# Kernel tuning notes

Hardware: AMD Instinct MI355X
Metric: run time of the kernel (lower is better)

Reference implementation:

```python
import jax, jax.numpy as jnp
import numpy as np

BETA = 0.25
N_E = 1024
E_DIM = 64
B, L = 32, 2048


def setup_inputs() -> dict:
    key = jax.random.key(0)
    k1, k2 = jax.random.split(key)
    z = jax.random.normal(k1, (B, L, E_DIM), dtype=jnp.float32)
    # torch init: uniform_(-1/n_e, 1/n_e)
    codebook = jax.random.uniform(k2, (N_E, E_DIM), dtype=jnp.float32,
                                  minval=-1.0 / N_E, maxval=1.0 / N_E)
    return {"z": z, "codebook": codebook}


def reference(z, codebook):
    sg = jax.lax.stop_gradient
    n_e = codebook.shape[0]
    zf = z.reshape(-1, codebook.shape[1])  # (N, e_dim)
    # squared-distance matrix: ||z||^2 + ||e||^2 - 2 z.e  -> (N, n_e)
    d = (jnp.sum(zf * zf, axis=1, keepdims=True)
         + jnp.sum(codebook * codebook, axis=1)
         - 2.0 * zf @ codebook.T)
    idx = jnp.argmin(d, axis=1)  # (N,)
    # one-hot @ codebook is just a gather
    z_q = codebook[idx].reshape(z.shape)
    loss = (jnp.mean((sg(z_q) - z) ** 2)
            + BETA * jnp.mean((z_q - sg(z)) ** 2))
    # straight-through estimator
    z_q_st = z + sg(z_q - z)
    # codebook usage stats (mean of one-hot rows == normalized histogram)
    counts = jnp.zeros((n_e,), dtype=z.dtype).at[idx].add(1.0)
    e_mean = counts / idx.shape[0]
    perplexity = jnp.exp(-jnp.sum(e_mean * jnp.log(e_mean + 1e-10)))
    return loss, z_q_st, perplexity, idx
```

## Files before the change

kernel.cpp:

```cpp
#include <hip/hip_runtime.h>
#include <math.h>

#define E_DIM 64
#define N_E   1024
#define BETA  0.25
#define NROWS 65536

using bf16x8 = __attribute__((ext_vector_type(8))) short;
using f32x4  = __attribute__((ext_vector_type(4))) float;
#define MFMA(a, b, c) __builtin_amdgcn_mfma_f32_16x16x32_bf16((a), (b), (c), 0, 0, 0)


__device__ __forceinline__ unsigned short f2bf_rn(float f) {
    unsigned u = __builtin_bit_cast(unsigned, f);
    unsigned r = u + 0x7fffu + ((u >> 16) & 1u);
    return (unsigned short)(r >> 16);
}
__device__ __forceinline__ float bf2f(unsigned short b) {
    unsigned u = ((unsigned)b) << 16;
    return __builtin_bit_cast(float, u);
}

__device__ __forceinline__ float pw64_sq(const float* v) {
    float r[8];
#pragma unroll
    for (int l = 0; l < 8; ++l) r[l] = v[l] * v[l];
#pragma unroll
    for (int t = 1; t < 8; ++t)
#pragma unroll
        for (int l = 0; l < 8; ++l) r[l] += v[8 * t + l] * v[8 * t + l];
    return ((r[0] + r[1]) + (r[2] + r[3])) + ((r[4] + r[5]) + (r[6] + r[7]));
}

__global__ __launch_bounds__(256) void k_prep(const float* __restrict__ cb,
                                              unsigned short* __restrict__ ebh,
                                              unsigned short* __restrict__ ebl,
                                              float* __restrict__ h,
                                              unsigned* __restrict__ hist,
                                              double* __restrict__ sse,
                                              unsigned* __restrict__ flagN) {
    int t = blockIdx.x * 256 + threadIdx.x;
    {
        int e = t & 7, lane = (t >> 3) & 63, ks = (t >> 9) & 1, ct = t >> 10;
        int j = ct * 16 + (lane & 15);
        int k = ks * 32 + ((lane >> 4) << 3) + e;
        float v = cb[j * 64 + k];
        unsigned short hi = f2bf_rn(v);
        ebh[t] = hi;
        ebl[t] = f2bf_rn(v - bf2f(hi));
    }
    if (blockIdx.x < 4) {
        int j = t;
        float e[E_DIM];
        const float4* ep = reinterpret_cast<const float4*>(cb + (size_t)j * E_DIM);
#pragma unroll
        for (int k4 = 0; k4 < E_DIM / 4; ++k4) {
            float4 v = ep[k4];
            e[4 * k4 + 0] = v.x; e[4 * k4 + 1] = v.y;
            e[4 * k4 + 2] = v.z; e[4 * k4 + 3] = v.w;
        }
        h[j] = pw64_sq(e);
    } else if (blockIdx.x == 4) {
#pragma unroll
        for (int u = 0; u < 4; ++u) hist[threadIdx.x * 4 + u] = 0u;
    } else if (blockIdx.x == 5 && threadIdx.x == 0) {
        *sse = 0.0;
        *flagN = 0u;
    }
}

__global__ __launch_bounds__(512, 4) void k_mfma(
    const float* __restrict__ z, const float* __restrict__ cb,
    const float* __restrict__ h,
    const unsigned short* __restrict__ ebh, const unsigned short* __restrict__ ebl,
    float* __restrict__ out_zq, float* __restrict__ out_idx,
    unsigned* __restrict__ hist, double* __restrict__ sse,
    unsigned* __restrict__ flagN, unsigned* __restrict__ flagL) {
    const int lane = threadIdx.x & 63;
    const int w = __builtin_amdgcn_readfirstlane(threadIdx.x >> 6);
    const int m = lane & 15, g = lane >> 4;
    const int half = w >> 2;
    const int rw   = w & 3;

    __shared__ int bok;
    __shared__ float rsv[128];
    __shared__ float sb0[2][128], sb1[2][128];
    __shared__ int   sbi[2][128];
    __shared__ float wp[8];
    if (threadIdx.x == 0) bok = 1;
    __syncthreads();

    {
        bf16x8 a, b;
#pragma unroll
        for (int e = 0; e < 8; ++e) {
            int k = g * 8 + e;
            a[e] = (short)f2bf_rn((float)(((m * 3 + k * 7) & 15) - 7));
            b[e] = (short)f2bf_rn((float)(((k * 5 + m * 3) & 15) - 8));
        }
        f32x4 acc = {0.f, 0.f, 0.f, 0.f};
        acc = MFMA(a, b, acc);
        bool ok = true;
#pragma unroll
        for (int r = 0; r < 4; ++r) {
            int rr = g * 4 + r;
            float E = 0.f;
            for (int k = 0; k < 32; ++k)
                E += (float)((((rr * 3 + k * 7) & 15) - 7) * (((k * 5 + m * 3) & 15) - 8));
            ok = ok && (acc[r] == E);
        }
        if (!ok) atomicAnd(&bok, 0);
    }
    __syncthreads();
    if (!bok) {
        if (threadIdx.x < 128) {
            unsigned p = atomicAdd(flagN, 1u);
            flagL[p] = (unsigned)(blockIdx.x * 128 + threadIdx.x);
        }
        return;
    }

    const int rowb32 = blockIdx.x * 128 + rw * 32;
    bf16x8 a0h0, a0l0, a0h1, a0l1, a1h0, a1l0, a1h1, a1l1;
#define ALOAD(P, AH0, AL0, AH1, AL1) {                                         \
        const int rowA = rowb32 + (P) * 16 + m;                                \
        const float4* zr = reinterpret_cast<const float4*>(z + (size_t)rowA * 64); \
        float4 p0 = zr[g * 2], p1 = zr[g * 2 + 1];                             \
        float4 p2 = zr[8 + g * 2], p3 = zr[9 + g * 2];                         \
        float t0[8] = {p0.x, p0.y, p0.z, p0.w, p1.x, p1.y, p1.z, p1.w};        \
        float t1[8] = {p2.x, p2.y, p2.z, p2.w, p3.x, p3.y, p3.z, p3.w};        \
        float s = 0.f;                                                         \
        _Pragma("unroll")                                                      \
        for (int e = 0; e < 8; ++e) {                                          \
            s += fabsf(t0[e]) + fabsf(t1[e]);                                  \
            float x0 = 2.0f * t0[e]; unsigned short h0 = f2bf_rn(x0);          \
            AH0[e] = (short)h0; AL0[e] = (short)f2bf_rn(x0 - bf2f(h0));        \
            float x1 = 2.0f * t1[e]; unsigned short h1 = f2bf_rn(x1);          \
            AH1[e] = (short)h1; AL1[e] = (short)f2bf_rn(x1 - bf2f(h1));        \
        }                                                                      \
        s += __shfl_xor(s, 16);                                                \
        s += __shfl_xor(s, 32);                                                \
        if (g == 0 && half == 0) rsv[rw * 32 + (P) * 16 + m] = s;              \
    }
    ALOAD(0, a0h0, a0l0, a0h1, a0l1)
    ALOAD(1, a1h0, a1l0, a1h1, a1l1)
#undef ALOAD

    float bb00 = INFINITY, bb01 = INFINITY, bb02 = INFINITY, bb03 = INFINITY;
    float bb10 = INFINITY, bb11 = INFINITY, bb12 = INFINITY, bb13 = INFINITY;
    float ss00 = INFINITY, ss01 = INFINITY, ss02 = INFINITY, ss03 = INFINITY;
    float ss10 = INFINITY, ss11 = INFINITY, ss12 = INFINITY, ss13 = INFINITY;
    int   ii00 = 0, ii01 = 0, ii02 = 0, ii03 = 0;
    int   ii10 = 0, ii11 = 0, ii12 = 0, ii13 = 0;
#define UPD(S, B0, B1, I0) { float _s = (S);                                   \
        if (_s < B0) { B1 = B0; B0 = _s; I0 = j; } else B1 = fminf(B1, _s); }

    const bf16x8* pBh = reinterpret_cast<const bf16x8*>(ebh);
    const bf16x8* pBl = reinterpret_cast<const bf16x8*>(ebl);
    const int ct0 = half * 32;

    bf16x8 Ah0 = pBh[ct0 * 128 + lane],        Ah1 = pBh[ct0 * 128 + lane + 64];
    bf16x8 Al0 = pBl[ct0 * 128 + lane],        Al1 = pBl[ct0 * 128 + lane + 64];
    bf16x8 Bh0 = pBh[(ct0 + 1) * 128 + lane],  Bh1 = pBh[(ct0 + 1) * 128 + lane + 64];
    bf16x8 Bl0 = pBl[(ct0 + 1) * 128 + lane],  Bl1 = pBl[(ct0 + 1) * 128 + lane + 64];

#define COLTILE(CT, VH0, VH1, VL0, VL1) {                                      \
        const int j = (CT) * 16 + m;                                           \
        const float hj = h[j];                                                 \
        const f32x4 z4 = {0.f, 0.f, 0.f, 0.f};                                 \
        f32x4 s0 = MFMA(a0h0, VH0, z4);                                        \
        f32x4 s1 = MFMA(a1h0, VH0, z4);                                        \
        s0 = MFMA(a0h1, VH1, s0);                                              \
        s1 = MFMA(a1h1, VH1, s1);                                              \
        s0 = MFMA(a0h0, VL0, s0);                                              \
        s1 = MFMA(a1h0, VL0, s1);                                              \
        s0 = MFMA(a0h1, VL1, s0);                                              \
        s1 = MFMA(a1h1, VL1, s1);                                              \
        s0 = MFMA(a0l0, VH0, s0);                                              \
        s1 = MFMA(a1l0, VH0, s1);                                              \
        s0 = MFMA(a0l1, VH1, s0);                                              \
        s1 = MFMA(a1l1, VH1, s1);                                              \
        UPD(hj - s0[0], bb00, ss00, ii00)                                      \
        UPD(hj - s0[1], bb01, ss01, ii01)                                      \
        UPD(hj - s0[2], bb02, ss02, ii02)                                      \
        UPD(hj - s0[3], bb03, ss03, ii03)                                      \
        UPD(hj - s1[0], bb10, ss10, ii10)                                      \
        UPD(hj - s1[1], bb11, ss11, ii11)                                      \
        UPD(hj - s1[2], bb12, ss12, ii12)                                      \
        UPD(hj - s1[3], bb13, ss13, ii13)                                      \
    }

#pragma unroll 1
    for (int ct = ct0; ct < ct0 + 32; ct += 2) {
        COLTILE(ct, Ah0, Ah1, Al0, Al1);
        if (ct + 2 < ct0 + 32) {
            const int fb = (ct + 2) * 128 + lane;
            Ah0 = pBh[fb]; Ah1 = pBh[fb + 64];
            Al0 = pBl[fb]; Al1 = pBl[fb + 64];
        }
        COLTILE(ct + 1, Bh0, Bh1, Bl0, Bl1);
        if (ct + 3 < ct0 + 32) {
            const int fb = (ct + 3) * 128 + lane;
            Bh0 = pBh[fb]; Bh1 = pBh[fb + 64];
            Bl0 = pBl[fb]; Bl1 = pBl[fb + 64];
        }
    }
#undef COLTILE
#undef UPD

#pragma unroll
    for (int mask = 1; mask < 16; mask <<= 1) {
#define MRG(B0, I0, B1) { float ob0 = __shfl_xor(B0, mask); int oi = __shfl_xor(I0, mask); \
        float ob1 = __shfl_xor(B1, mask); \
        if (ob0 < B0) { B1 = fminf(fminf(B0, B1), ob1); B0 = ob0; I0 = oi; } \
        else { B1 = fminf(B1, fminf(ob0, ob1)); } }
        MRG(bb00, ii00, ss00) MRG(bb01, ii01, ss01)
        MRG(bb02, ii02, ss02) MRG(bb03, ii03, ss03)
        MRG(bb10, ii10, ss10) MRG(bb11, ii11, ss11)
        MRG(bb12, ii12, ss12) MRG(bb13, ii13, ss13)
#undef MRG
    }

    if (m == 0) {
        const int r0 = rw * 32 + g * 4;
        sb0[half][r0 + 0] = bb00; sb1[half][r0 + 0] = ss00; sbi[half][r0 + 0] = ii00;
        sb0[half][r0 + 1] = bb01; sb1[half][r0 + 1] = ss01; sbi[half][r0 + 1] = ii01;
        sb0[half][r0 + 2] = bb02; sb1[half][r0 + 2] = ss02; sbi[half][r0 + 2] = ii02;
        sb0[half][r0 + 3] = bb03; sb1[half][r0 + 3] = ss03; sbi[half][r0 + 3] = ii03;
        const int r1 = r0 + 16;
        sb0[half][r1 + 0] = bb10; sb1[half][r1 + 0] = ss10; sbi[half][r1 + 0] = ii10;
        sb0[half][r1 + 1] = bb11; sb1[half][r1 + 1] = ss11; sbi[half][r1 + 1] = ii11;
        sb0[half][r1 + 2] = bb12; sb1[half][r1 + 2] = ss12; sbi[half][r1 + 2] = ii12;
        sb0[half][r1 + 3] = bb13; sb1[half][r1 + 3] = ss13; sbi[half][r1 + 3] = ii13;
    }
    __syncthreads();

    {
        const int rloc = threadIdx.x >> 2, q = threadIdx.x & 3;
        const int rowO = blockIdx.x * 128 + rloc;
        float b0 = sb0[0][rloc], b1 = sb1[0][rloc];
        int   vi = sbi[0][rloc];
        {
            float c0 = sb0[1][rloc], c1 = sb1[1][rloc];
            int   ci = sbi[1][rloc];
            if (c0 < b0) { b1 = fminf(b0, c1); b0 = c0; vi = ci; }
            else         { b1 = fminf(b1, c0); }
        }
        const float Delta = 6e-8f * rsv[rloc] + 2.2e-5f;
        float local = 0.f;
        if (b1 - b0 <= Delta) {
            if (q == 0) { unsigned p = atomicAdd(flagN, 1u); flagL[p] = (unsigned)rowO; }
        } else {
            if (q == 0) { out_idx[rowO] = (float)vi; atomicAdd(&hist[vi], 1u); }
            const float4* cv = reinterpret_cast<const float4*>(cb + (size_t)vi * 64) + q * 4;
            const float4* zv = reinterpret_cast<const float4*>(z + (size_t)rowO * 64) + q * 4;
            float* orow = out_zq + (size_t)rowO * 64 + q * 16;
#pragma unroll
            for (int u = 0; u < 4; ++u) {
                float4 cc = cv[u], zo = zv[u];
                orow[4 * u + 0] = cc.x; orow[4 * u + 1] = cc.y;
                orow[4 * u + 2] = cc.z; orow[4 * u + 3] = cc.w;
                float dx = cc.x - zo.x, dy = cc.y - zo.y;
                float dz = cc.z - zo.z, dw = cc.w - zo.w;
                local = fmaf(dx, dx, local); local = fmaf(dy, dy, local);
                local = fmaf(dz, dz, local); local = fmaf(dw, dw, local);
            }
        }
#pragma unroll
        for (int off = 32; off; off >>= 1) local += __shfl_down(local, off);
        if (lane == 0) wp[w] = local;
    }
    __syncthreads();
    if (threadIdx.x == 0) {
        float t = ((wp[0] + wp[1]) + (wp[2] + wp[3]))
                + ((wp[4] + wp[5]) + (wp[6] + wp[7]));
        atomicAdd(sse, (double)t);
    }
}

__global__ __launch_bounds__(64, 4) void k_cleanup(
    const float* __restrict__ z, const float* __restrict__ cb,
    const float* __restrict__ h,
    const unsigned* __restrict__ flagN, const unsigned* __restrict__ flagL,
    float* __restrict__ out_zq, float* __restrict__ out_idx,
    unsigned* __restrict__ hist, double* __restrict__ sse) {
    const unsigned n = *flagN;
    const int lane = threadIdx.x;

    for (unsigned f = blockIdx.x; f < n; f += gridDim.x) {
        const int row = (int)flagL[f];

        float tz[E_DIM];
        const float4* zp = reinterpret_cast<const float4*>(z + (size_t)row * 64);
#pragma unroll
        for (int k4 = 0; k4 < 16; ++k4) {
            float4 v = zp[k4];
            tz[4 * k4 + 0] = v.x; tz[4 * k4 + 1] = v.y;
            tz[4 * k4 + 2] = v.z; tz[4 * k4 + 3] = v.w;
        }
        const float nz = pw64_sq(tz);
#pragma unroll
        for (int k = 0; k < 64; ++k) tz[k] = 2.0f * tz[k];

        float bs = INFINITY;
        int bj = 0;
#pragma unroll 2
        for (int t = 0; t < 16; ++t) {
            const int j = lane + 64 * t;
            const float4* cv = reinterpret_cast<const float4*>(cb + (size_t)j * 64);
            float mm = 0.f;
#pragma unroll
            for (int k4 = 0; k4 < 16; ++k4) {
                float4 e = cv[k4];
                mm = fmaf(tz[4 * k4 + 0], e.x, mm);
                mm = fmaf(tz[4 * k4 + 1], e.y, mm);
                mm = fmaf(tz[4 * k4 + 2], e.z, mm);
                mm = fmaf(tz[4 * k4 + 3], e.w, mm);
            }
            float sc = (nz + h[j]) - mm;
            if (sc < bs) { bs = sc; bj = j; }
        }
#pragma unroll
        for (int off = 32; off; off >>= 1) {
            float s2 = __shfl_down(bs, off);
            int   j2 = __shfl_down(bj, off);
            if (s2 < bs || (s2 == bs && j2 < bj)) { bs = s2; bj = j2; }
        }
        bj = __shfl(bj, 0);

        float c = cb[(size_t)bj * 64 + lane];
        out_zq[(size_t)row * 64 + lane] = c;
        float d = c - 0.5f * tz[lane];
        float l2 = d * d;
#pragma unroll
        for (int off = 32; off; off >>= 1) l2 += __shfl_down(l2, off);
        if (lane == 0) {
            out_idx[row] = (float)bj;
            atomicAdd(&hist[bj], 1u);
            atomicAdd(sse, (double)l2);
        }
    }
}

__global__ __launch_bounds__(256) void k_h_fb(const float* __restrict__ cb,
                                              float* __restrict__ h) {
    int j = blockIdx.x * 256 + threadIdx.x;
    if (j < N_E) {
        float e[E_DIM];
        const float4* ep = reinterpret_cast<const float4*>(cb + (size_t)j * E_DIM);
#pragma unroll
        for (int k4 = 0; k4 < E_DIM / 4; ++k4) {
            float4 v = ep[k4];
            e[4 * k4 + 0] = v.x; e[4 * k4 + 1] = v.y;
            e[4 * k4 + 2] = v.z; e[4 * k4 + 3] = v.w;
        }
        h[j] = pw64_sq(e);
    }
}

__global__ __launch_bounds__(512, 2) void k_scan_fb(
    const float* __restrict__ z, const float* __restrict__ cb,
    const float* __restrict__ h,
    float* __restrict__ out_zq, float* __restrict__ out_idx,
    unsigned* __restrict__ hist, double* __restrict__ sse) {
    const int lane = threadIdx.x & 63;
    const int w = __builtin_amdgcn_readfirstlane(threadIdx.x >> 6);
    const int row = blockIdx.x * 64 + lane;
    float tz[E_DIM];
    const float4* zp = reinterpret_cast<const float4*>(z + (size_t)row * E_DIM);
#pragma unroll
    for (int k4 = 0; k4 < E_DIM / 4; ++k4) {
        float4 v = zp[k4];
        tz[4 * k4 + 0] = v.x; tz[4 * k4 + 1] = v.y;
        tz[4 * k4 + 2] = v.z; tz[4 * k4 + 3] = v.w;
    }
    const float nz = pw64_sq(tz);
#pragma unroll
    for (int k = 0; k < E_DIM; ++k) tz[k] = 2.0f * tz[k];
    float b0 = INFINITY; int bi = 0;
    const int j0 = w * 128;
#pragma unroll 1
    for (int j = j0; j < j0 + 128; j += 4) {
        const float* c0 = cb + (size_t)j * E_DIM;
        float m0 = 0.f, m1 = 0.f, m2 = 0.f, m3 = 0.f;
#pragma unroll
        for (int k = 0; k < E_DIM; ++k) {
            float wk = tz[k];
            m0 = fmaf(wk, c0[0 * E_DIM + k], m0);
            m1 = fmaf(wk, c0[1 * E_DIM + k], m1);
            m2 = fmaf(wk, c0[2 * E_DIM + k], m2);
            m3 = fmaf(wk, c0[3 * E_DIM + k], m3);
        }
        float s0 = (nz + h[j + 0]) - m0;
        float s1 = (nz + h[j + 1]) - m1;
        float s2 = (nz + h[j + 2]) - m2;
        float s3 = (nz + h[j + 3]) - m3;
        if (s0 < b0) { b0 = s0; bi = j + 0; }
        if (s1 < b0) { b0 = s1; bi = j + 1; }
        if (s2 < b0) { b0 = s2; bi = j + 2; }
        if (s3 < b0) { b0 = s3; bi = j + 3; }
    }
    __shared__ float lb[8][64];
    __shared__ int   li[8][64];
    lb[w][lane] = b0; li[w][lane] = bi;
    __syncthreads();
    if (threadIdx.x < 64) {
        float b = lb[0][lane]; int i = li[0][lane];
#pragma unroll
        for (int c = 1; c < 8; ++c) {
            float bc = lb[c][lane]; int ic = li[c][lane];
            if (bc < b) { b = bc; i = ic; }
        }
        out_idx[row] = (float)i;
        float local = 0.f;
        const float4* cv = reinterpret_cast<const float4*>(cb + (size_t)i * E_DIM);
        float* orow = out_zq + (size_t)row * E_DIM;
#pragma unroll
        for (int k4 = 0; k4 < E_DIM / 4; ++k4) {
            float4 c = cv[k4];
            float zx = 0.5f * tz[4 * k4 + 0], zy = 0.5f * tz[4 * k4 + 1];
            float zz = 0.5f * tz[4 * k4 + 2], zw = 0.5f * tz[4 * k4 + 3];
            orow[4 * k4 + 0] = c.x; orow[4 * k4 + 1] = c.y;
            orow[4 * k4 + 2] = c.z; orow[4 * k4 + 3] = c.w;
            float dx = c.x - zx, dy = c.y - zy, dz = c.z - zz, dw = c.w - zw;
            local = fmaf(dx, dx, local); local = fmaf(dy, dy, local);
            local = fmaf(dz, dz, local); local = fmaf(dw, dw, local);
        }
        atomicAdd(&hist[i], 1u);
#pragma unroll
        for (int off = 32; off; off >>= 1) local += __shfl_down(local, off);
        if (lane == 0) atomicAdd(sse, (double)local);
    }
}

__global__ __launch_bounds__(256) void k_final(
    const unsigned* __restrict__ hist, const double* __restrict__ sse,
    float* __restrict__ out, int nrows) {
    __shared__ double sh[256];
    double acc = 0.0;
    for (int j = threadIdx.x; j < N_E; j += 256) {
        double p = (double)hist[j] / (double)nrows;
        acc += p * log(p + 1e-10);
    }
    sh[threadIdx.x] = acc;
    __syncthreads();
    for (int s = 128; s; s >>= 1) {
        if (threadIdx.x < s) sh[threadIdx.x] += sh[threadIdx.x + s];
        __syncthreads();
    }
    if (threadIdx.x == 0) {
        double ntot = (double)nrows * (double)E_DIM;
        out[0] = (float)((1.0 + BETA) * (*sse) / ntot);
        out[1 + (size_t)nrows * E_DIM] = (float)exp(-sh[0]);
    }
}

extern "C" void kernel_launch(void* const* d_in, const int* in_sizes, int n_in,
                              void* d_out, int out_size, void* d_ws, size_t ws_size,
                              hipStream_t stream) {
    const float* z  = (const float*)d_in[0];
    const float* cb = (const float*)d_in[1];
    const int nrows = in_sizes[0] / E_DIM;
    float* out = (float*)d_out;

    char* ws = (char*)d_ws;
    unsigned* hist  = (unsigned*)(ws + 0);
    double*   sse   = (double*)  (ws + 4096);
    unsigned* flagN = (unsigned*)(ws + 4104);
    float*    h     = (float*)   (ws + 4112);
    unsigned short* ebh = (unsigned short*)(ws + 8208);
    unsigned short* ebl = (unsigned short*)(ws + 139280);
    unsigned* flagL = (unsigned*)(ws + 270352);

    float* out_zq  = out + 1;
    float* out_idx = out + 1 + (size_t)nrows * E_DIM + 1;

    if (ws_size >= 532496) {
        k_prep<<<256, 256, 0, stream>>>(cb, ebh, ebl, h, hist, sse, flagN);
        k_mfma<<<nrows / 128, 512, 0, stream>>>(z, cb, h, ebh, ebl,
                                                out_zq, out_idx, hist, sse,
                                                flagN, flagL);
        k_cleanup<<<2048, 64, 0, stream>>>(z, cb, h, flagN, flagL,
                                           out_zq, out_idx, hist, sse);
    } else {
        hipMemsetAsync(d_ws, 0, 4112, stream);
        k_h_fb<<<(N_E + 255) / 256, 256, 0, stream>>>(cb, h);
        k_scan_fb<<<nrows / 64, 512, 0, stream>>>(z, cb, h, out_zq, out_idx, hist, sse);
    }
    k_final<<<1, 256, 0, stream>>>(hist, sse, out, nrows);
}
```

Measured before the change: 102.8 us.

## Deepen codebook prefetch, stage norms in LDS, fuse final reduction into cleanup

The MFMA scan loop now keeps four codebook tiles in registers instead of two, so loads are issued further ahead of their use. The codebook norms are first copied into shared memory, which removes per-tile global loads of h. The separate single-block final kernel is removed: the last cleanup block to finish, chosen by an atomic counter, computes loss and perplexity. This saves one launch, but the extra live registers may lower occupancy under the (512,4) launch bound.

Result: slower. 229.4 us (+123.2%).

```diff
diff --git a/kernel.cpp b/kernel.cpp
--- a/kernel.cpp
+++ b/kernel.cpp
@@ -38,7 +38,8 @@
                                               float* __restrict__ h,
                                               unsigned* __restrict__ hist,
                                               double* __restrict__ sse,
-                                              unsigned* __restrict__ flagN) {
+                                              unsigned* __restrict__ flagN,
+                                              unsigned* __restrict__ done) {
     int t = blockIdx.x * 256 + threadIdx.x;
     {
         int e = t & 7, lane = (t >> 3) & 63, ks = (t >> 9) & 1, ct = t >> 10;
@@ -66,6 +67,7 @@
     } else if (blockIdx.x == 5 && threadIdx.x == 0) {
         *sse = 0.0;
         *flagN = 0u;
+        *done = 0u;
     }
 }
 
@@ -83,11 +85,13 @@
     const int rw   = w & 3;
 
     __shared__ int bok;
+    __shared__ float sh_h[N_E];
     __shared__ float rsv[128];
     __shared__ float sb0[2][128], sb1[2][128];
     __shared__ int   sbi[2][128];
     __shared__ float wp[8];
     if (threadIdx.x == 0) bok = 1;
+    for (int i = threadIdx.x; i < N_E; i += 512) sh_h[i] = h[i];
     __syncthreads();
 
     {
@@ -159,14 +163,19 @@
     const bf16x8* pBl = reinterpret_cast<const bf16x8*>(ebl);
     const int ct0 = half * 32;
 
-    bf16x8 Ah0 = pBh[ct0 * 128 + lane],        Ah1 = pBh[ct0 * 128 + lane + 64];
-    bf16x8 Al0 = pBl[ct0 * 128 + lane],        Al1 = pBl[ct0 * 128 + lane + 64];
-    bf16x8 Bh0 = pBh[(ct0 + 1) * 128 + lane],  Bh1 = pBh[(ct0 + 1) * 128 + lane + 64];
-    bf16x8 Bl0 = pBl[(ct0 + 1) * 128 + lane],  Bl1 = pBl[(ct0 + 1) * 128 + lane + 64];
+    bf16x8 S0h0, S0h1, S0l0, S0l1, S1h0, S1h1, S1l0, S1l1;
+    bf16x8 S2h0, S2h1, S2l0, S2l1, S3h0, S3h1, S3l0, S3l1;
+#define LOADSET(SET, CT) { const int fb = (CT) * 128 + lane;                   \
+        SET##h0 = pBh[fb]; SET##h1 = pBh[fb + 64];                             \
+        SET##l0 = pBl[fb]; SET##l1 = pBl[fb + 64]; }
+    LOADSET(S0, ct0)
+    LOADSET(S1, ct0 + 1)
+    LOADSET(S2, ct0 + 2)
+    LOADSET(S3, ct0 + 3)
 
 #define COLTILE(CT, VH0, VH1, VL0, VL1) {                                      \
         const int j = (CT) * 16 + m;                                           \
-        const float hj = h[j];                                                 \
+        const float hj = sh_h[j];                                              \
         const f32x4 z4 = {0.f, 0.f, 0.f, 0.f};                                 \
         f32x4 s0 = MFMA(a0h0, VH0, z4);                                        \
         f32x4 s1 = MFMA(a1h0, VH0, z4);                                        \
@@ -191,21 +200,18 @@
     }
 
 #pragma unroll 1
-    for (int ct = ct0; ct < ct0 + 32; ct += 2) {
-        COLTILE(ct, Ah0, Ah1, Al0, Al1);
-        if (ct + 2 < ct0 + 32) {
-            const int fb = (ct + 2) * 128 + lane;
-            Ah0 = pBh[fb]; Ah1 = pBh[fb + 64];
-            Al0 = pBl[fb]; Al1 = pBl[fb + 64];
-        }
-        COLTILE(ct + 1, Bh0, Bh1, Bl0, Bl1);
-        if (ct + 3 < ct0 + 32) {
-            const int fb = (ct + 3) * 128 + lane;
-            Bh0 = pBh[fb]; Bh1 = pBh[fb + 64];
-            Bl0 = pBl[fb]; Bl1 = pBl[fb + 64];
-        }
+    for (int ct = ct0; ct < ct0 + 32; ct += 4) {
+        COLTILE(ct, S0h0, S0h1, S0l0, S0l1);
+        if (ct + 4 < ct0 + 32) LOADSET(S0, ct + 4)
+        COLTILE(ct + 1, S1h0, S1h1, S1l0, S1l1);
+        if (ct + 5 < ct0 + 32) LOADSET(S1, ct + 5)
+        COLTILE(ct + 2, S2h0, S2h1, S2l0, S2l1);
+        if (ct + 6 < ct0 + 32) LOADSET(S2, ct + 6)
+        COLTILE(ct + 3, S3h0, S3h1, S3l0, S3l1);
+        if (ct + 7 < ct0 + 32) LOADSET(S3, ct + 7)
     }
 #undef COLTILE
+#undef LOADSET
 #undef UPD
 
 #pragma unroll
@@ -283,7 +289,8 @@
     const float* __restrict__ h,
     const unsigned* __restrict__ flagN, const unsigned* __restrict__ flagL,
     float* __restrict__ out_zq, float* __restrict__ out_idx,
-    unsigned* __restrict__ hist, double* __restrict__ sse) {
+    unsigned* __restrict__ hist, double* __restrict__ sse,
+    unsigned* __restrict__ done, float* __restrict__ out, int nrows) {
     const unsigned n = *flagN;
     const int lane = threadIdx.x;
 
@@ -338,6 +345,30 @@
             out_idx[row] = (float)bj;
             atomicAdd(&hist[bj], 1u);
             atomicAdd(sse, (double)l2);
+        }
+    }
+
+    __shared__ int last;
+    if (lane == 0) {
+        __threadfence();
+        unsigned d = atomicAdd(done, 1u);
+        last = (d == gridDim.x - 1) ? 1 : 0;
+    }
+    __syncthreads();
+    if (last) {
+        double acc = 0.0;
+        for (int j = lane; j < N_E; j += 64) {
+            unsigned c = atomicAdd(&hist[j], 0u);
+            double p = (double)c / (double)nrows;
+            acc += p * log(p + 1e-10);
+        }
+#pragma unroll
+        for (int off = 32; off; off >>= 1) acc += __shfl_down(acc, off);
+        if (lane == 0) {
+            double sv = atomicAdd(sse, 0.0);
+            double ntot = (double)nrows * 64.0;
+            out[0] = (float)((1.0 + BETA) * sv / ntot);
+            out[1 + (size_t)nrows * 64] = (float)exp(-acc);
         }
     }
 }
@@ -467,6 +498,7 @@
     unsigned* hist  = (unsigned*)(ws + 0);
     double*   sse   = (double*)  (ws + 4096);
     unsigned* flagN = (unsigned*)(ws + 4104);
+    unsigned* done  = (unsigned*)(ws + 4108);
     float*    h     = (float*)   (ws + 4112);
     unsigned short* ebh = (unsigned short*)(ws + 8208);
     unsigned short* ebl = (unsigned short*)(ws + 139280);
@@ -476,16 +508,17 @@
     float* out_idx = out + 1 + (size_t)nrows * E_DIM + 1;
 
     if (ws_size >= 532496) {
-        k_prep<<<256, 256, 0, stream>>>(cb, ebh, ebl, h, hist, sse, flagN);
+        k_prep<<<256, 256, 0, stream>>>(cb, ebh, ebl, h, hist, sse, flagN, done);
         k_mfma<<<nrows / 128, 512, 0, stream>>>(z, cb, h, ebh, ebl,
                                                 out_zq, out_idx, hist, sse,
                                                 flagN, flagL);
         k_cleanup<<<2048, 64, 0, stream>>>(z, cb, h, flagN, flagL,
-                                           out_zq, out_idx, hist, sse);
+                                           out_zq, out_idx, hist, sse,
+                                           done, out, nrows);
     } else {
         hipMemsetAsync(d_ws, 0, 4112, stream);
         k_h_fb<<<(N_E + 255) / 256, 256, 0, stream>>>(cb, h);
         k_scan_fb<<<nrows / 64, 512, 0, stream>>>(z, cb, h, out_zq, out_idx, hist, sse);
-    }
-    k_final<<<1, 256, 0, stream>>>(hist, sse, out, nrows);
-}
+        k_final<<<1, 256, 0, stream>>>(hist, sse, out, nrows);
+    }
+}
```
